# Performance work log

Measured on AMD Instinct MI355X. Metric: run time of the kernel, lower is better.

The kernel has to match this reference:

```python
import jax, jax.numpy as jnp
import numpy as np

B, S, H = 2, 2048, 4096          # batch, seq_len, hidden_size
NH, NKV, D = 32, 8, 128          # query heads, kv heads (GQA), head_dim
WINDOW = 1024                    # sliding window size
EPS = 1e-5
THETA = 10000.0


def setup_inputs() -> dict:
    key = jax.random.key(0)
    ks = jax.random.split(key, 5)
    w = lambda k, shape: jax.random.normal(k, shape, jnp.float32) * 0.02
    return {
        "hidden_states": jax.random.normal(ks[0], (B, S, H), jnp.float32),
        "wq": w(ks[1], (H, NH * D)),
        "wk": w(ks[2], (H, NKV * D)),
        "wv": w(ks[3], (H, NKV * D)),
        "wo": w(ks[4], (NH * D, H)),
        "q_norm_w": jnp.ones((D,), jnp.float32),
        "k_norm_w": jnp.ones((D,), jnp.float32),
    }


def _rmsnorm(x, w):
    # Exaone4RMSNorm over the last (head_dim) axis
    var = jnp.mean(jnp.square(x.astype(jnp.float32)), axis=-1, keepdims=True)
    return (x * jax.lax.rsqrt(var + EPS)).astype(x.dtype) * w


def _rotate_half(x):
    x1, x2 = jnp.split(x, 2, axis=-1)
    return jnp.concatenate([-x2, x1], axis=-1)


def reference(hidden_states, wq, wk, wv, wo, q_norm_w, k_norm_w):
    # QKV projections (no bias)
    q = (hidden_states @ wq).reshape(B, S, NH, D)
    k = (hidden_states @ wk).reshape(B, S, NKV, D)
    v = (hidden_states @ wv).reshape(B, S, NKV, D)
    # per-head QK RMSNorm, then [B, h, S, D] layout
    q = _rmsnorm(q, q_norm_w).transpose(0, 2, 1, 3)
    k = _rmsnorm(k, k_norm_w).transpose(0, 2, 1, 3)
    v = v.transpose(0, 2, 1, 3)
    # RoPE (applied on sliding-window layers in EXAONE4)
    pos = jnp.arange(S)
    inv_freq = 1.0 / (THETA ** (jnp.arange(0, D, 2, dtype=jnp.float32) / D))
    freqs = pos[:, None].astype(jnp.float32) * inv_freq[None, :]   # [S, D/2]
    emb = jnp.concatenate([freqs, freqs], axis=-1)                 # [S, D]
    cos, sin = jnp.cos(emb), jnp.sin(emb)
    q = q * cos + _rotate_half(q) * sin
    k = k * cos + _rotate_half(k) * sin
    # GQA: repeat kv heads to match query heads
    k = jnp.repeat(k, NH // NKV, axis=1)
    v = jnp.repeat(v, NH // NKV, axis=1)
    # SDPA with causal sliding-window mask: q_pos - WINDOW < k_pos <= q_pos
    scores = jnp.einsum('bhqd,bhkd->bhqk', q, k) / jnp.sqrt(jnp.float32(D))
    diff = pos[:, None] - pos[None, :]
    mask = (diff >= 0) & (diff < WINDOW)
    scores = jnp.where(mask, scores, jnp.finfo(scores.dtype).min)
    probs = jax.nn.softmax(scores, axis=-1)
    out = jnp.einsum('bhqk,bhkd->bhqd', probs, v)
    out = out.transpose(0, 2, 1, 3).reshape(B, S, NH * D)
    return out @ wo
```

## Files before the change

### kernel.cpp

```cpp
#include <hip/hip_runtime.h>
#include <hip/hip_bf16.h>

#define B_ 2
#define S_ 2048
#define H_ 4096
#define NH_ 32
#define NKV_ 8
#define D_ 128
#define WINDOW_ 1024
#define EPS_ 1e-5f
#define M_ (B_*S_)
#define NQKV_ ((NH_ + 2*NKV_) * D_)

typedef __attribute__((ext_vector_type(8))) __bf16 bf16x8;
typedef __attribute__((ext_vector_type(4))) float f32x4;
typedef __attribute__((ext_vector_type(16))) float f32x16;

__device__ __forceinline__ unsigned short f2bf(float f) {
  union { __hip_bfloat16 h; unsigned short us; } cv;
  cv.h = __float2bfloat16(f);
  return cv.us;
}
__device__ __forceinline__ float bf2f(unsigned short u) {
  union { __hip_bfloat16 h; unsigned short us; } cv;
  cv.us = u;
  return __bfloat162float(cv.h);
}

__device__ __forceinline__ void gload16(const unsigned short* g, unsigned short* l) {
  __builtin_amdgcn_global_load_lds(
      (const __attribute__((address_space(1))) unsigned int*)(const void*)g,
      (__attribute__((address_space(3))) unsigned int*)(void*)l, 16, 0, 0);
}

__global__ __launch_bounds__(256) void transpose_convert(
    const float* __restrict__ in, unsigned short* __restrict__ out, int K, int N) {
  __shared__ float tile[32][33];
  const int n0 = blockIdx.x * 32, k0 = blockIdx.y * 32;
  const int t = threadIdx.x;
  #pragma unroll
  for (int i = 0; i < 4; ++i) {
    int e = i * 256 + t; int r = e >> 5, c = e & 31;
    tile[r][c] = in[(size_t)(k0 + r) * N + n0 + c];
  }
  __syncthreads();
  #pragma unroll
  for (int i = 0; i < 4; ++i) {
    int e = i * 256 + t; int r = e >> 5, c = e & 31;
    out[(size_t)(n0 + r) * K + k0 + c] = f2bf(tile[c][r]);
  }
}

__global__ __launch_bounds__(256) void convert_bf16_kernel(
    const float* __restrict__ in, unsigned short* __restrict__ out, int n4) {
  int i = blockIdx.x * 256 + threadIdx.x;
  if (i >= n4) return;
  float4 v = ((const float4*)in)[i];
  ushort4 o;
  o.x = f2bf(v.x); o.y = f2bf(v.y); o.z = f2bf(v.z); o.w = f2bf(v.w);
  ((ushort4*)out)[i] = o;
}

template <bool OUT_BF16>
__global__ __launch_bounds__(512) void gemm256(
    const unsigned short* __restrict__ A, const unsigned short* __restrict__ Bt,
    void* __restrict__ Cout, int N, int K) {
  __shared__ __align__(16) unsigned short lds[2][2][16384];
  const int tid = threadIdx.x;
  const int wave = tid >> 6, lane = tid & 63;
  const int l15 = lane & 15, l16 = lane >> 4;
  const int m0 = blockIdx.y * 256, n0 = blockIdx.x * 256;
  const int wmi = wave >> 2, wni = wave & 3;

  const unsigned short* asrc[4];
  const unsigned short* bsrc[4];
  #pragma unroll
  for (int it = 0; it < 4; ++it) {
    const int d = it * 512 + tid;
    const int row = d >> 3, ci = d & 7;
    const int cis = ci ^ (row & 7);
    asrc[it] = A + (size_t)(m0 + row) * K + cis * 8;
    bsrc[it] = Bt + (size_t)(n0 + row) * K + cis * 8;
  }

  f32x4 acc[8][4];
  #pragma unroll
  for (int mi = 0; mi < 8; ++mi)
    #pragma unroll
    for (int ni = 0; ni < 4; ++ni) acc[mi][ni] = (f32x4){0.f, 0.f, 0.f, 0.f};

#define STAGE256(buf, kt)                                              \
  { _Pragma("unroll") for (int it = 0; it < 4; ++it) {                 \
      const int dst = it * 4096 + wave * 512;                          \
      gload16(asrc[it] + (size_t)(kt) * 64, &lds[buf][0][dst]);        \
      gload16(bsrc[it] + (size_t)(kt) * 64, &lds[buf][1][dst]);        \
    } }

  const int nk = K >> 6;
  STAGE256(0, 0)
  for (int t = 0; t < nk; ++t) {
    const int cur = t & 1;
    if (t + 1 < nk) {
      STAGE256(cur ^ 1, t + 1)
      asm volatile("s_waitcnt vmcnt(8)" ::: "memory");
    } else {
      asm volatile("s_waitcnt vmcnt(0)" ::: "memory");
    }
    __builtin_amdgcn_s_barrier();
    __builtin_amdgcn_sched_barrier(0);
    const unsigned short* as = lds[cur][0];
    const unsigned short* bs = lds[cur][1];
    #pragma unroll
    for (int kk = 0; kk < 2; ++kk) {
      bf16x8 af[8], bfv[4];
      #pragma unroll
      for (int mi = 0; mi < 8; ++mi) {
        const int row = wmi * 128 + mi * 16 + l15;
        af[mi] = *(const bf16x8*)&as[row * 64 + ((kk * 4 + l16) ^ (row & 7)) * 8];
      }
      #pragma unroll
      for (int ni = 0; ni < 4; ++ni) {
        const int row = wni * 64 + ni * 16 + l15;
        bfv[ni] = *(const bf16x8*)&bs[row * 64 + ((kk * 4 + l16) ^ (row & 7)) * 8];
      }
      asm volatile("s_waitcnt lgkmcnt(0)" ::: "memory");
      __builtin_amdgcn_sched_barrier(0);
      __builtin_amdgcn_s_setprio(1);
      #pragma unroll
      for (int mi = 0; mi < 8; ++mi)
        #pragma unroll
        for (int ni = 0; ni < 4; ++ni)
          acc[mi][ni] = __builtin_amdgcn_mfma_f32_16x16x32_bf16(af[mi], bfv[ni], acc[mi][ni], 0, 0, 0);
      __builtin_amdgcn_s_setprio(0);
    }
    __builtin_amdgcn_s_barrier();
    __builtin_amdgcn_sched_barrier(0);
  }
#undef STAGE256

  #pragma unroll
  for (int mi = 0; mi < 8; ++mi) {
    #pragma unroll
    for (int ni = 0; ni < 4; ++ni) {
      const int col = n0 + wni * 64 + ni * 16 + l15;
      #pragma unroll
      for (int j = 0; j < 4; ++j) {
        const int row = m0 + wmi * 128 + mi * 16 + l16 * 4 + j;
        if (OUT_BF16)
          ((unsigned short*)Cout)[(size_t)row * N + col] = f2bf(acc[mi][ni][j]);
        else
          ((float*)Cout)[(size_t)row * N + col] = acc[mi][ni][j];
      }
    }
  }
}

__global__ __launch_bounds__(256) void norm_rope_kernel(
    const unsigned short* __restrict__ QKVg,
    const float* __restrict__ qw, const float* __restrict__ kw,
    unsigned short* __restrict__ Qr, unsigned short* __restrict__ Kr) {
  const int bs = blockIdx.x;
  const int b = bs >> 11, s = bs & (S_ - 1);
  const int wave = threadIdx.x >> 6, lane = threadIdx.x & 63;

  float invf = 1.0f / powf(10000.0f, (float)lane * (1.0f / 64.0f));
  float sn, cs;
  sincosf((float)s * invf, &sn, &cs);

  const unsigned short* row = QKVg + (size_t)bs * NQKV_;
  const float qwa = qw[lane], qwb = qw[lane + 64];
  const float kwa = kw[lane], kwb = kw[lane + 64];
  const float scale = 0.08838834764831845f;

  for (int h = wave; h < NH_; h += 4) {
    float x0 = bf2f(row[h * D_ + lane]);
    float x1 = bf2f(row[h * D_ + 64 + lane]);
    float ss = x0 * x0 + x1 * x1;
    #pragma unroll
    for (int o = 32; o >= 1; o >>= 1) ss += __shfl_xor(ss, o);
    float r = rsqrtf(ss * (1.0f / 128.0f) + EPS_);
    x0 *= r * qwa; x1 *= r * qwb;
    float o0 = (x0 * cs - x1 * sn) * scale;
    float o1 = (x1 * cs + x0 * sn) * scale;
    size_t off = (((size_t)b * NH_ + h) * S_ + s) * D_;
    Qr[off + lane] = f2bf(o0);
    Qr[off + 64 + lane] = f2bf(o1);
  }
  for (int h = wave; h < NKV_; h += 4) {
    float x0 = bf2f(row[NH_ * D_ + h * D_ + lane]);
    float x1 = bf2f(row[NH_ * D_ + h * D_ + 64 + lane]);
    float ss = x0 * x0 + x1 * x1;
    #pragma unroll
    for (int o = 32; o >= 1; o >>= 1) ss += __shfl_xor(ss, o);
    float r = rsqrtf(ss * (1.0f / 128.0f) + EPS_);
    x0 *= r * kwa; x1 *= r * kwb;
    float o0 = x0 * cs - x1 * sn;
    float o1 = x1 * cs + x0 * sn;
    size_t off = (((size_t)b * NKV_ + h) * S_ + s) * D_;
    Kr[off + lane] = f2bf(o0);
    Kr[off + 64 + lane] = f2bf(o1);
  }
}

__global__ __launch_bounds__(256) void vtrans_kernel(
    const unsigned short* __restrict__ QKVg, unsigned short* __restrict__ Vt) {
  __shared__ unsigned short t[64][65];
  const int s0 = blockIdx.x * 64, d0 = blockIdx.y * 64;
  const int bh = blockIdx.z;
  const int b = bh >> 3, hk = bh & 7;
  const int tid = threadIdx.x;
  #pragma unroll
  for (int i = 0; i < 16; ++i) {
    int e = i * 256 + tid; int sr = e >> 6, dc = e & 63;
    t[sr][dc] = QKVg[(size_t)(b * S_ + s0 + sr) * NQKV_ + (NH_ + NKV_) * D_ + hk * D_ + d0 + dc];
  }
  __syncthreads();
  #pragma unroll
  for (int i = 0; i < 16; ++i) {
    int e = i * 256 + tid; int dr = e >> 6, sc = e & 63;
    Vt[((size_t)bh * D_ + d0 + dr) * S_ + s0 + sc] = t[sc][dr];
  }
}

__global__ __launch_bounds__(512) void attn_kernel(
    const unsigned short* __restrict__ Qr, const unsigned short* __restrict__ Kr,
    const unsigned short* __restrict__ Vt, unsigned short* __restrict__ Out) {
  const int q0 = blockIdx.x * 256;
  const int h = blockIdx.y, b = blockIdx.z, hk = h >> 2;
  const int tid = threadIdx.x;
  const int wave = tid >> 6, lane = tid & 63;
  const int l31 = lane & 31, hi = lane >> 5;
  const int qw0 = q0 + wave * 32;
  const int qpos = qw0 + l31;

  __shared__ __align__(16) unsigned short Ks[64 * 128];
  __shared__ __align__(16) unsigned short Vs[128 * 64];

  bf16x8 qf[8];
  {
    const unsigned short* qp = Qr + (((size_t)b * NH_ + h) * S_ + qpos) * D_ + hi * 8;
    #pragma unroll
    for (int ds = 0; ds < 8; ++ds) qf[ds] = *(const bf16x8*)(qp + ds * 16);
  }

  f32x16 o[4];
  #pragma unroll
  for (int i = 0; i < 4; ++i)
    #pragma unroll
    for (int j = 0; j < 16; ++j) o[i][j] = 0.f;
  float mrun = -1e30f, lrun = 0.f;

  const size_t kbase = ((size_t)b * NKV_ + hk) * S_;
  const size_t vbase = ((size_t)b * NKV_ + hk) * D_;

  const int ktlo = (q0 > 1023) ? ((q0 - 1023) & ~63) : 0;
  const int kthi = (q0 + 255) & ~63;
  const int wlo = (qw0 > 1023) ? ((qw0 - 1023) & ~63) : 0;
  const int whi = (qw0 + 31) & ~63;

  for (int kt = ktlo; kt <= kthi; kt += 64) {
    __syncthreads();
    #pragma unroll
    for (int it = 0; it < 2; ++it) {
      const int cb = it * 512 + wave * 64;
      const int c = cb + lane;
      const int rk = c >> 4, sk = c & 15;
      gload16(Kr + (kbase + kt + rk) * D_ + ((sk ^ (rk & 7)) * 8), Ks + (size_t)cb * 8);
      const int rv = c >> 3, sv = c & 7;
      gload16(Vt + (vbase + rv) * S_ + kt + ((sv ^ (rv & 7)) * 8), Vs + (size_t)cb * 8);
    }
    __syncthreads();
    if (kt < wlo || kt > whi) continue;

    f32x16 s0, s1;
    #pragma unroll
    for (int j = 0; j < 16; ++j) { s0[j] = 0.f; s1[j] = 0.f; }
    __builtin_amdgcn_s_setprio(1);
    #pragma unroll
    for (int ds = 0; ds < 8; ++ds) {
      const int g = ((ds * 2 + hi) ^ (l31 & 7)) * 8;
      bf16x8 k0 = *(const bf16x8*)&Ks[l31 * 128 + g];
      bf16x8 k1 = *(const bf16x8*)&Ks[(l31 + 32) * 128 + g];
      s0 = __builtin_amdgcn_mfma_f32_32x32x16_bf16(k0, qf[ds], s0, 0, 0, 0);
      s1 = __builtin_amdgcn_mfma_f32_32x32x16_bf16(k1, qf[ds], s1, 0, 0, 0);
    }
    __builtin_amdgcn_s_setprio(0);

    const bool fullValid = (kt + 63 <= qw0) && (kt >= qw0 - 992);
    if (!fullValid) {
      const int d0 = qpos - kt;
      #pragma unroll
      for (int r = 0; r < 16; ++r) {
        const int koff = (r & 3) + 8 * (r >> 2) + 4 * hi;
        if ((unsigned)(d0 - koff) >= (unsigned)WINDOW_) s0[r] = -1e30f;
        if ((unsigned)(d0 - koff - 32) >= (unsigned)WINDOW_) s1[r] = -1e30f;
      }
    }

    float pm = -1e30f;
    #pragma unroll
    for (int r = 0; r < 16; ++r) pm = fmaxf(pm, fmaxf(s0[r], s1[r]));
    pm = fmaxf(pm, __shfl_xor(pm, 32));
    const float mnew = fmaxf(mrun, pm);
    const float scl = __expf(mrun - mnew);
    mrun = mnew;
    float ts = 0.f;
    #pragma unroll
    for (int r = 0; r < 16; ++r) {
      s0[r] = __expf(s0[r] - mnew); ts += s0[r];
      s1[r] = __expf(s1[r] - mnew); ts += s1[r];
    }
    ts += __shfl_xor(ts, 32);
    lrun = lrun * scl + ts;
    #pragma unroll
    for (int i = 0; i < 4; ++i)
      #pragma unroll
      for (int j = 0; j < 16; ++j) o[i][j] *= scl;

    unsigned pw[2][2][4];
    #pragma unroll
    for (int t2 = 0; t2 < 2; ++t2) {
      const f32x16 sv = t2 ? s1 : s0;
      #pragma unroll
      for (int sub = 0; sub < 2; ++sub) {
        const int bs4 = sub * 8;
        unsigned A0 = ((unsigned)f2bf(sv[bs4 + 1]) << 16) | f2bf(sv[bs4 + 0]);
        unsigned A1 = ((unsigned)f2bf(sv[bs4 + 3]) << 16) | f2bf(sv[bs4 + 2]);
        unsigned B0 = ((unsigned)f2bf(sv[bs4 + 5]) << 16) | f2bf(sv[bs4 + 4]);
        unsigned B1 = ((unsigned)f2bf(sv[bs4 + 7]) << 16) | f2bf(sv[bs4 + 6]);
        unsigned sA0 = __shfl_xor(A0, 32), sA1 = __shfl_xor(A1, 32);
        unsigned sB0 = __shfl_xor(B0, 32), sB1 = __shfl_xor(B1, 32);
        pw[t2][sub][0] = hi ? sB0 : A0;
        pw[t2][sub][1] = hi ? sB1 : A1;
        pw[t2][sub][2] = hi ? B0 : sA0;
        pw[t2][sub][3] = hi ? B1 : sA1;
      }
    }

    __builtin_amdgcn_s_setprio(1);
    #pragma unroll
    for (int t2 = 0; t2 < 2; ++t2)
      #pragma unroll
      for (int sub = 0; sub < 2; ++sub) {
        union { unsigned u[4]; bf16x8 v; } pb;
        pb.u[0] = pw[t2][sub][0]; pb.u[1] = pw[t2][sub][1];
        pb.u[2] = pw[t2][sub][2]; pb.u[3] = pw[t2][sub][3];
        #pragma unroll
        for (int dt = 0; dt < 4; ++dt) {
          const int rr = dt * 32 + l31;
          const int g = ((t2 * 4 + sub * 2 + hi) ^ (rr & 7)) * 8;
          bf16x8 vf = *(const bf16x8*)&Vs[rr * 64 + g];
          o[dt] = __builtin_amdgcn_mfma_f32_32x32x16_bf16(vf, pb.v, o[dt], 0, 0, 0);
        }
      }
    __builtin_amdgcn_s_setprio(0);
  }

  const float inv = 1.0f / lrun;
  unsigned short* op = Out + (size_t)(b * S_ + qpos) * (NH_ * D_) + h * D_;
  #pragma unroll
  for (int dt = 0; dt < 4; ++dt)
    #pragma unroll
    for (int g = 0; g < 4; ++g) {
      const int r = g * 4;
      uint2 val;
      val.x = ((unsigned)f2bf(o[dt][r + 1] * inv) << 16) | f2bf(o[dt][r + 0] * inv);
      val.y = ((unsigned)f2bf(o[dt][r + 3] * inv) << 16) | f2bf(o[dt][r + 2] * inv);
      *(uint2*)(op + dt * 32 + 8 * g + 4 * hi) = val;
    }
}

extern "C" void kernel_launch(void* const* d_in, const int* in_sizes, int n_in,
                              void* d_out, int out_size, void* d_ws, size_t ws_size,
                              hipStream_t stream) {
  const float* hidden = (const float*)d_in[0];
  const float* wq = (const float*)d_in[1];
  const float* wk = (const float*)d_in[2];
  const float* wv = (const float*)d_in[3];
  const float* wo = (const float*)d_in[4];
  const float* qw = (const float*)d_in[5];
  const float* kw = (const float*)d_in[6];
  float* out = (float*)d_out;

  char* ws = (char*)d_ws;
  unsigned short* wqkv = (unsigned short*)(ws);
  unsigned short* kr   = (unsigned short*)(ws);
  unsigned short* vt   = (unsigned short*)(ws + ((size_t)8 << 20));
  unsigned short* attn = (unsigned short*)(ws + ((size_t)16 << 20));
  unsigned short* qkvg = (unsigned short*)(ws + ((size_t)48 << 20));
  unsigned short* wot  = (unsigned short*)(ws + ((size_t)48 << 20));
  unsigned short* hb   = (unsigned short*)d_out;
  unsigned short* qr   = (unsigned short*)d_out + ((size_t)16 << 20);

  transpose_convert<<<dim3(NH_ * D_ / 32, H_ / 32), 256, 0, stream>>>(wq, wqkv, H_, NH_ * D_);
  transpose_convert<<<dim3(NKV_ * D_ / 32, H_ / 32), 256, 0, stream>>>(
      wk, wqkv + (size_t)NH_ * D_ * H_, H_, NKV_ * D_);
  transpose_convert<<<dim3(NKV_ * D_ / 32, H_ / 32), 256, 0, stream>>>(
      wv, wqkv + (size_t)(NH_ + NKV_) * D_ * H_, H_, NKV_ * D_);

  convert_bf16_kernel<<<(M_ * H_ / 4 + 255) / 256, 256, 0, stream>>>(hidden, hb, M_ * H_ / 4);

  gemm256<true><<<dim3(NQKV_ / 256, M_ / 256), 512, 0, stream>>>(hb, wqkv, qkvg, NQKV_, H_);

  norm_rope_kernel<<<M_, 256, 0, stream>>>(qkvg, qw, kw, qr, kr);

  vtrans_kernel<<<dim3(S_ / 64, D_ / 64, B_ * NKV_), 256, 0, stream>>>(qkvg, vt);

  transpose_convert<<<dim3(H_ / 32, H_ / 32), 256, 0, stream>>>(wo, wot, NH_ * D_, H_);

  attn_kernel<<<dim3(S_ / 256, NH_, B_), 512, 0, stream>>>(qr, kr, vt, attn);

  gemm256<false><<<dim3(H_ / 256, M_ / 256), 512, 0, stream>>>(attn, wot, out, H_, H_);
}
```

Measured before the change: 550.6 us.

## Shrink GEMM tile to 256x128, remap blocks across XCDs, split LDS reads

The GEMM tile shrinks from 256x256 to 256x128, which doubles the block count for the QKV and output projections (more blocks across 256 CUs, less LDS per block). Block IDs are remapped so consecutive logical tiles land on the same XCD for L2 reuse. Fragment loads for the two k-halves are issued up front, with a partial lgkmcnt wait so the first MFMA batch can overlap the second batch's LDS reads. The trade-off is lower arithmetic intensity per tile and more global traffic for A.

```diff
diff --git a/kernel.cpp b/kernel.cpp
--- a/kernel.cpp
+++ b/kernel.cpp
@@ -65,84 +65,111 @@
 __global__ __launch_bounds__(512) void gemm256(
     const unsigned short* __restrict__ A, const unsigned short* __restrict__ Bt,
     void* __restrict__ Cout, int N, int K) {
-  __shared__ __align__(16) unsigned short lds[2][2][16384];
+  __shared__ __align__(16) unsigned short lds[2][24576];
   const int tid = threadIdx.x;
   const int wave = tid >> 6, lane = tid & 63;
   const int l15 = lane & 15, l16 = lane >> 4;
-  const int m0 = blockIdx.y * 256, n0 = blockIdx.x * 256;
+
+  const int nwg = gridDim.x * gridDim.y;
+  const int bid = blockIdx.y * gridDim.x + blockIdx.x;
+  const int wg = (bid & 7) * (nwg >> 3) + (bid >> 3);
+  const int m0 = (wg / gridDim.x) * 256;
+  const int n0 = (wg % gridDim.x) * 128;
   const int wmi = wave >> 2, wni = wave & 3;
 
   const unsigned short* asrc[4];
-  const unsigned short* bsrc[4];
+  const unsigned short* bsrc[2];
   #pragma unroll
   for (int it = 0; it < 4; ++it) {
     const int d = it * 512 + tid;
-    const int row = d >> 3, ci = d & 7;
-    const int cis = ci ^ (row & 7);
+    const int row = d >> 3, cis = (d & 7) ^ (row & 7);
     asrc[it] = A + (size_t)(m0 + row) * K + cis * 8;
+  }
+  #pragma unroll
+  for (int it = 0; it < 2; ++it) {
+    const int d = it * 512 + tid;
+    const int row = d >> 3, cis = (d & 7) ^ (row & 7);
     bsrc[it] = Bt + (size_t)(n0 + row) * K + cis * 8;
   }
 
-  f32x4 acc[8][4];
+  f32x4 acc[8][2];
   #pragma unroll
   for (int mi = 0; mi < 8; ++mi)
     #pragma unroll
-    for (int ni = 0; ni < 4; ++ni) acc[mi][ni] = (f32x4){0.f, 0.f, 0.f, 0.f};
-
-#define STAGE256(buf, kt)                                              \
-  { _Pragma("unroll") for (int it = 0; it < 4; ++it) {                 \
-      const int dst = it * 4096 + wave * 512;                          \
-      gload16(asrc[it] + (size_t)(kt) * 64, &lds[buf][0][dst]);        \
-      gload16(bsrc[it] + (size_t)(kt) * 64, &lds[buf][1][dst]);        \
-    } }
+    for (int ni = 0; ni < 2; ++ni) acc[mi][ni] = (f32x4){0.f, 0.f, 0.f, 0.f};
+
+#define STG(buf, kt)                                                        \
+  { _Pragma("unroll") for (int it = 0; it < 4; ++it)                        \
+      gload16(asrc[it] + (size_t)(kt) * 64, &lds[buf][(it * 512 + wave * 64) * 8]); \
+    _Pragma("unroll") for (int it = 0; it < 2; ++it)                        \
+      gload16(bsrc[it] + (size_t)(kt) * 64, &lds[buf][16384 + (it * 512 + wave * 64) * 8]); }
 
   const int nk = K >> 6;
-  STAGE256(0, 0)
+  STG(0, 0)
   for (int t = 0; t < nk; ++t) {
     const int cur = t & 1;
     if (t + 1 < nk) {
-      STAGE256(cur ^ 1, t + 1)
-      asm volatile("s_waitcnt vmcnt(8)" ::: "memory");
+      STG(cur ^ 1, t + 1)
+      asm volatile("s_waitcnt vmcnt(6)" ::: "memory");
     } else {
       asm volatile("s_waitcnt vmcnt(0)" ::: "memory");
     }
+    __builtin_amdgcn_sched_barrier(0);
     __builtin_amdgcn_s_barrier();
     __builtin_amdgcn_sched_barrier(0);
-    const unsigned short* as = lds[cur][0];
-    const unsigned short* bs = lds[cur][1];
-    #pragma unroll
-    for (int kk = 0; kk < 2; ++kk) {
-      bf16x8 af[8], bfv[4];
-      #pragma unroll
-      for (int mi = 0; mi < 8; ++mi) {
-        const int row = wmi * 128 + mi * 16 + l15;
-        af[mi] = *(const bf16x8*)&as[row * 64 + ((kk * 4 + l16) ^ (row & 7)) * 8];
-      }
-      #pragma unroll
-      for (int ni = 0; ni < 4; ++ni) {
-        const int row = wni * 64 + ni * 16 + l15;
-        bfv[ni] = *(const bf16x8*)&bs[row * 64 + ((kk * 4 + l16) ^ (row & 7)) * 8];
-      }
-      asm volatile("s_waitcnt lgkmcnt(0)" ::: "memory");
-      __builtin_amdgcn_sched_barrier(0);
-      __builtin_amdgcn_s_setprio(1);
-      #pragma unroll
-      for (int mi = 0; mi < 8; ++mi)
-        #pragma unroll
-        for (int ni = 0; ni < 4; ++ni)
-          acc[mi][ni] = __builtin_amdgcn_mfma_f32_16x16x32_bf16(af[mi], bfv[ni], acc[mi][ni], 0, 0, 0);
-      __builtin_amdgcn_s_setprio(0);
-    }
+    const unsigned short* as = lds[cur];
+    const unsigned short* bs = lds[cur] + 16384;
+    bf16x8 a0[8], b0[2], a1[8], b1[2];
+    #pragma unroll
+    for (int mi = 0; mi < 8; ++mi) {
+      const int row = wmi * 128 + mi * 16 + l15;
+      a0[mi] = *(const bf16x8*)&as[row * 64 + (l16 ^ (row & 7)) * 8];
+    }
+    #pragma unroll
+    for (int ni = 0; ni < 2; ++ni) {
+      const int row = wni * 32 + ni * 16 + l15;
+      b0[ni] = *(const bf16x8*)&bs[row * 64 + (l16 ^ (row & 7)) * 8];
+    }
+    __builtin_amdgcn_sched_barrier(0);
+    #pragma unroll
+    for (int mi = 0; mi < 8; ++mi) {
+      const int row = wmi * 128 + mi * 16 + l15;
+      a1[mi] = *(const bf16x8*)&as[row * 64 + ((4 + l16) ^ (row & 7)) * 8];
+    }
+    #pragma unroll
+    for (int ni = 0; ni < 2; ++ni) {
+      const int row = wni * 32 + ni * 16 + l15;
+      b1[ni] = *(const bf16x8*)&bs[row * 64 + ((4 + l16) ^ (row & 7)) * 8];
+    }
+    asm volatile("s_waitcnt lgkmcnt(10)" ::: "memory");
+    __builtin_amdgcn_sched_barrier(0);
+    __builtin_amdgcn_s_setprio(1);
+    #pragma unroll
+    for (int mi = 0; mi < 8; ++mi)
+      #pragma unroll
+      for (int ni = 0; ni < 2; ++ni)
+        acc[mi][ni] = __builtin_amdgcn_mfma_f32_16x16x32_bf16(a0[mi], b0[ni], acc[mi][ni], 0, 0, 0);
+    __builtin_amdgcn_s_setprio(0);
+    asm volatile("s_waitcnt lgkmcnt(0)" ::: "memory");
+    __builtin_amdgcn_sched_barrier(0);
+    __builtin_amdgcn_s_setprio(1);
+    #pragma unroll
+    for (int mi = 0; mi < 8; ++mi)
+      #pragma unroll
+      for (int ni = 0; ni < 2; ++ni)
+        acc[mi][ni] = __builtin_amdgcn_mfma_f32_16x16x32_bf16(a1[mi], b1[ni], acc[mi][ni], 0, 0, 0);
+    __builtin_amdgcn_s_setprio(0);
+    __builtin_amdgcn_sched_barrier(0);
     __builtin_amdgcn_s_barrier();
     __builtin_amdgcn_sched_barrier(0);
   }
-#undef STAGE256
+#undef STG
 
   #pragma unroll
   for (int mi = 0; mi < 8; ++mi) {
     #pragma unroll
-    for (int ni = 0; ni < 4; ++ni) {
-      const int col = n0 + wni * 64 + ni * 16 + l15;
+    for (int ni = 0; ni < 2; ++ni) {
+      const int col = n0 + wni * 32 + ni * 16 + l15;
       #pragma unroll
       for (int j = 0; j < 4; ++j) {
         const int row = m0 + wmi * 128 + mi * 16 + l16 * 4 + j;
@@ -400,7 +427,7 @@
 
   convert_bf16_kernel<<<(M_ * H_ / 4 + 255) / 256, 256, 0, stream>>>(hidden, hb, M_ * H_ / 4);
 
-  gemm256<true><<<dim3(NQKV_ / 256, M_ / 256), 512, 0, stream>>>(hb, wqkv, qkvg, NQKV_, H_);
+  gemm256<true><<<dim3(NQKV_ / 128, M_ / 256), 512, 0, stream>>>(hb, wqkv, qkvg, NQKV_, H_);
 
   norm_rope_kernel<<<M_, 256, 0, stream>>>(qkvg, qw, kw, qr, kr);
 
@@ -410,5 +437,5 @@
 
   attn_kernel<<<dim3(S_ / 256, NH_, B_), 512, 0, stream>>>(qr, kr, vt, attn);
 
-  gemm256<false><<<dim3(H_ / 256, M_ / 256), 512, 0, stream>>>(attn, wot, out, H_, H_);
-}
+  gemm256<false><<<dim3(H_ / 128, M_ / 256), 512, 0, stream>>>(attn, wot, out, H_, H_);
+}
```

New measurement: 564.0 us. 2.4% more time.

## Switch GEMM to 32x32x16 MFMA with pipelined LDS reads across k-groups

Applied to the files above, without the earlier changes.

Both projection GEMMs now issue 32x32x16 bf16 MFMAs on 32x32 fragments instead of 16x16x32 ones. This cuts the number of MFMA instructions and LDS fragment loads for the same 256x256 block tile. The inner k-tile is split into four k=16 groups, and LDS reads for the next group are issued before the MFMAs of the current group, with partial lgkmcnt waits, so LDS latency overlaps with matrix math. The epilogue index mapping changes to match the 32x32 accumulator layout, which risks correctness if the row mapping is wrong.

```diff
diff --git a/kernel.cpp b/kernel.cpp
--- a/kernel.cpp
+++ b/kernel.cpp
@@ -62,13 +62,13 @@
 }
 
 template <bool OUT_BF16>
-__global__ __launch_bounds__(512) void gemm256(
+__global__ __launch_bounds__(512) void gemm32(
     const unsigned short* __restrict__ A, const unsigned short* __restrict__ Bt,
     void* __restrict__ Cout, int N, int K) {
   __shared__ __align__(16) unsigned short lds[2][2][16384];
   const int tid = threadIdx.x;
   const int wave = tid >> 6, lane = tid & 63;
-  const int l15 = lane & 15, l16 = lane >> 4;
+  const int l31 = lane & 31, hi = lane >> 5;
   const int m0 = blockIdx.y * 256, n0 = blockIdx.x * 256;
   const int wmi = wave >> 2, wni = wave & 3;
 
@@ -77,79 +77,97 @@
   #pragma unroll
   for (int it = 0; it < 4; ++it) {
     const int d = it * 512 + tid;
-    const int row = d >> 3, ci = d & 7;
-    const int cis = ci ^ (row & 7);
+    const int row = d >> 3, cis = (d & 7) ^ (row & 7);
     asrc[it] = A + (size_t)(m0 + row) * K + cis * 8;
     bsrc[it] = Bt + (size_t)(n0 + row) * K + cis * 8;
   }
 
-  f32x4 acc[8][4];
-  #pragma unroll
-  for (int mi = 0; mi < 8; ++mi)
-    #pragma unroll
-    for (int ni = 0; ni < 4; ++ni) acc[mi][ni] = (f32x4){0.f, 0.f, 0.f, 0.f};
-
-#define STAGE256(buf, kt)                                              \
-  { _Pragma("unroll") for (int it = 0; it < 4; ++it) {                 \
-      const int dst = it * 4096 + wave * 512;                          \
-      gload16(asrc[it] + (size_t)(kt) * 64, &lds[buf][0][dst]);        \
-      gload16(bsrc[it] + (size_t)(kt) * 64, &lds[buf][1][dst]);        \
+  f32x16 acc[4][2];
+  #pragma unroll
+  for (int mi = 0; mi < 4; ++mi)
+    #pragma unroll
+    for (int ni = 0; ni < 2; ++ni)
+      #pragma unroll
+      for (int r = 0; r < 16; ++r) acc[mi][ni][r] = 0.f;
+
+#define STG(buf, kt)                                                         \
+  { _Pragma("unroll") for (int it = 0; it < 4; ++it) {                       \
+      const int dst = it * 4096 + wave * 512;                                \
+      gload16(asrc[it] + (size_t)(kt) * 64, &lds[buf][0][dst]);              \
+      gload16(bsrc[it] + (size_t)(kt) * 64, &lds[buf][1][dst]);              \
     } }
 
+#define READGRP(kk)                                                          \
+  { _Pragma("unroll") for (int mi = 0; mi < 4; ++mi) {                       \
+      const int r = wmi * 128 + mi * 32 + l31;                               \
+      a[kk][mi] = *(const bf16x8*)&as[r * 64 + (((kk)*2 + hi) ^ (r & 7)) * 8]; \
+    }                                                                        \
+    _Pragma("unroll") for (int ni = 0; ni < 2; ++ni) {                       \
+      const int r = wni * 64 + ni * 32 + l31;                                \
+      b[kk][ni] = *(const bf16x8*)&bs[r * 64 + (((kk)*2 + hi) ^ (r & 7)) * 8]; \
+    } }                                                                      \
+  __builtin_amdgcn_sched_barrier(0);
+
+#define MFMAGRP(kk)                                                          \
+  __builtin_amdgcn_s_setprio(1);                                             \
+  _Pragma("unroll") for (int mi = 0; mi < 4; ++mi)                           \
+    _Pragma("unroll") for (int ni = 0; ni < 2; ++ni)                         \
+      acc[mi][ni] = __builtin_amdgcn_mfma_f32_32x32x16_bf16(                 \
+          a[kk][mi], b[kk][ni], acc[mi][ni], 0, 0, 0);                       \
+  __builtin_amdgcn_s_setprio(0);
+
   const int nk = K >> 6;
-  STAGE256(0, 0)
+  STG(0, 0)
   for (int t = 0; t < nk; ++t) {
     const int cur = t & 1;
     if (t + 1 < nk) {
-      STAGE256(cur ^ 1, t + 1)
+      STG(cur ^ 1, t + 1)
       asm volatile("s_waitcnt vmcnt(8)" ::: "memory");
     } else {
       asm volatile("s_waitcnt vmcnt(0)" ::: "memory");
     }
+    __builtin_amdgcn_sched_barrier(0);
     __builtin_amdgcn_s_barrier();
     __builtin_amdgcn_sched_barrier(0);
     const unsigned short* as = lds[cur][0];
     const unsigned short* bs = lds[cur][1];
-    #pragma unroll
-    for (int kk = 0; kk < 2; ++kk) {
-      bf16x8 af[8], bfv[4];
-      #pragma unroll
-      for (int mi = 0; mi < 8; ++mi) {
-        const int row = wmi * 128 + mi * 16 + l15;
-        af[mi] = *(const bf16x8*)&as[row * 64 + ((kk * 4 + l16) ^ (row & 7)) * 8];
-      }
-      #pragma unroll
-      for (int ni = 0; ni < 4; ++ni) {
-        const int row = wni * 64 + ni * 16 + l15;
-        bfv[ni] = *(const bf16x8*)&bs[row * 64 + ((kk * 4 + l16) ^ (row & 7)) * 8];
-      }
-      asm volatile("s_waitcnt lgkmcnt(0)" ::: "memory");
-      __builtin_amdgcn_sched_barrier(0);
-      __builtin_amdgcn_s_setprio(1);
-      #pragma unroll
-      for (int mi = 0; mi < 8; ++mi)
-        #pragma unroll
-        for (int ni = 0; ni < 4; ++ni)
-          acc[mi][ni] = __builtin_amdgcn_mfma_f32_16x16x32_bf16(af[mi], bfv[ni], acc[mi][ni], 0, 0, 0);
-      __builtin_amdgcn_s_setprio(0);
-    }
+    bf16x8 a[4][4], b[4][2];
+    READGRP(0)
+    READGRP(1)
+    asm volatile("s_waitcnt lgkmcnt(6)" ::: "memory");
+    __builtin_amdgcn_sched_barrier(0);
+    MFMAGRP(0)
+    READGRP(2)
+    asm volatile("s_waitcnt lgkmcnt(6)" ::: "memory");
+    __builtin_amdgcn_sched_barrier(0);
+    MFMAGRP(1)
+    READGRP(3)
+    asm volatile("s_waitcnt lgkmcnt(6)" ::: "memory");
+    __builtin_amdgcn_sched_barrier(0);
+    MFMAGRP(2)
+    asm volatile("s_waitcnt lgkmcnt(0)" ::: "memory");
+    __builtin_amdgcn_sched_barrier(0);
+    MFMAGRP(3)
+    __builtin_amdgcn_sched_barrier(0);
     __builtin_amdgcn_s_barrier();
     __builtin_amdgcn_sched_barrier(0);
   }
-#undef STAGE256
-
-  #pragma unroll
-  for (int mi = 0; mi < 8; ++mi) {
-    #pragma unroll
-    for (int ni = 0; ni < 4; ++ni) {
-      const int col = n0 + wni * 64 + ni * 16 + l15;
-      #pragma unroll
-      for (int j = 0; j < 4; ++j) {
-        const int row = m0 + wmi * 128 + mi * 16 + l16 * 4 + j;
+#undef STG
+#undef READGRP
+#undef MFMAGRP
+
+  #pragma unroll
+  for (int mi = 0; mi < 4; ++mi) {
+    #pragma unroll
+    for (int ni = 0; ni < 2; ++ni) {
+      const int col = n0 + wni * 64 + ni * 32 + l31;
+      #pragma unroll
+      for (int r = 0; r < 16; ++r) {
+        const int row = m0 + wmi * 128 + mi * 32 + (r & 3) + 8 * (r >> 2) + 4 * hi;
         if (OUT_BF16)
-          ((unsigned short*)Cout)[(size_t)row * N + col] = f2bf(acc[mi][ni][j]);
+          ((unsigned short*)Cout)[(size_t)row * N + col] = f2bf(acc[mi][ni][r]);
         else
-          ((float*)Cout)[(size_t)row * N + col] = acc[mi][ni][j];
+          ((float*)Cout)[(size_t)row * N + col] = acc[mi][ni][r];
       }
     }
   }
@@ -400,7 +418,7 @@
 
   convert_bf16_kernel<<<(M_ * H_ / 4 + 255) / 256, 256, 0, stream>>>(hidden, hb, M_ * H_ / 4);
 
-  gemm256<true><<<dim3(NQKV_ / 256, M_ / 256), 512, 0, stream>>>(hb, wqkv, qkvg, NQKV_, H_);
+  gemm32<true><<<dim3(NQKV_ / 256, M_ / 256), 512, 0, stream>>>(hb, wqkv, qkvg, NQKV_, H_);
 
   norm_rope_kernel<<<M_, 256, 0, stream>>>(qkvg, qw, kw, qr, kr);
 
@@ -410,5 +428,5 @@
 
   attn_kernel<<<dim3(S_ / 256, NH_, B_), 512, 0, stream>>>(qr, kr, vt, attn);
 
-  gemm256<false><<<dim3(H_ / 256, M_ / 256), 512, 0, stream>>>(attn, wot, out, H_, H_);
-}
+  gemm32<false><<<dim3(H_ / 256, M_ / 256), 512, 0, stream>>>(attn, wot, out, H_, H_);
+}
```

Measured after the change: 570.2 us. 1.04x slower.
